# Kernel optimization log

Measured on AMD Instinct MI355X. Metric: run time of the kernel, lower is better.

The kernel has to match this reference:

```python
import jax, jax.numpy as jnp
import numpy as np


def _unfold(x, kh, kw):
    # torch.nn.functional.unfold ordering: channel-major, then kernel row, then kernel col
    B, C, H, W = x.shape
    Ho, Wo = H - kh + 1, W - kw + 1
    cols = jnp.stack([x[:, :, i:i + Ho, j:j + Wo]
                      for i in range(kh) for j in range(kw)], axis=2)  # [B,C,kh*kw,Ho,Wo]
    return cols.reshape(B, C * kh * kw, Ho * Wo), Ho, Wo


def _conv_unfold_matmul(x, w, b):
    # preprocessing: unfold -> A [B,L,K], B = w.view(O,-1).T [K,O]
    # matmul -> [B,L,O]; postprocessing: transpose, reshape, add bias
    O = w.shape[0]
    kh, kw = w.shape[2], w.shape[3]
    cols, Ho, Wo = _unfold(x, kh, kw)                      # [B,K,L]
    out = jnp.einsum('bkl,ok->bol', cols, w.reshape(O, -1))  # [B,O,L]
    return out.reshape(x.shape[0], O, Ho, Wo) + b[None, :, None, None]


def setup_inputs() -> dict:
    key = jax.random.key(0)
    ks = jax.random.split(key, 9)
    B = 4096
    x = jax.random.normal(ks[0], (B, 1, 28, 28), dtype=jnp.float32)
    w1 = jax.random.normal(ks[1], (10, 1, 10, 10), dtype=jnp.float32) * 0.1
    b1 = jax.random.normal(ks[2], (10,), dtype=jnp.float32) * 0.1
    w2 = jax.random.normal(ks[3], (20, 10, 10, 10), dtype=jnp.float32) * 0.03
    b2 = jax.random.normal(ks[4], (20,), dtype=jnp.float32) * 0.1
    w3 = jax.random.normal(ks[5], (20, 20, 5, 5), dtype=jnp.float32) * 0.04
    b3 = jax.random.normal(ks[6], (20,), dtype=jnp.float32) * 0.1
    wf = jax.random.normal(ks[7], (10, 720), dtype=jnp.float32) * 0.04
    bf = jax.random.normal(ks[8], (10,), dtype=jnp.float32) * 0.1
    return {"x": x, "w1": w1, "b1": b1, "w2": w2, "b2": b2,
            "w3": w3, "b3": b3, "wf": wf, "bf": bf}


def reference(x, w1, b1, w2, b2, w3, b3, wf, bf):
    h = jax.nn.relu(_conv_unfold_matmul(x, w1, b1))   # [B,10,19,19]
    h = jax.nn.relu(_conv_unfold_matmul(h, w2, b2))   # [B,20,10,10]
    h = jax.nn.relu(_conv_unfold_matmul(h, w3, b3))   # [B,20,6,6]
    h = h.reshape(-1, 720)
    return h @ wf.T + bf                               # [B,10]
```

## Files before the change

kernel.cpp:

```cpp
#include <hip/hip_runtime.h>


typedef short s16x4 __attribute__((ext_vector_type(4)));
typedef short s16x8 __attribute__((ext_vector_type(8)));
typedef float f32x4 __attribute__((ext_vector_type(4)));

#define ROW1 248
#define ROW2 248
#define XOFF 4712
#define SM_BYTES 11024

static __device__ __forceinline__ unsigned short f2bf(float f) {
    union { float f; unsigned int u; } v; v.f = f;
    unsigned int u = v.u;
    unsigned int r = (u + 0x7fffu + ((u >> 16) & 1u)) >> 16;
    return (unsigned short)r;
}

static __device__ __forceinline__ s16x8 cat8(s16x4 lo, s16x4 hi) {
    return __builtin_shufflevector(lo, hi, 0, 1, 2, 3, 4, 5, 6, 7);
}

__global__ __launch_bounds__(256) void wprep_k(const float* __restrict__ w1,
                                               const float* __restrict__ w2,
                                               const float* __restrict__ w3,
                                               unsigned short* __restrict__ wbuf) {
    int e = blockIdx.x * 256 + threadIdx.x;
    if (e < 40960) {
        int t = e & 7, lane = (e >> 3) & 63, nt = (e >> 9) & 1;
        int ck = (e >> 10) & 3, i = e >> 12;
        int k = ck * 32 + ((lane >> 4) & 3) * 8 + t;
        int o = nt * 16 + (lane & 15);
        int j = k / 12, c = k % 12;
        float val = (j < 10 && c < 10 && o < 20) ? w2[o * 1000 + c * 100 + i * 10 + j] : 0.f;
        wbuf[e] = f2bf(val);
    } else if (e < 61440) {
        int e2 = e - 40960;
        int t = e2 & 7, lane = (e2 >> 3) & 63, nt = (e2 >> 9) & 1;
        int ck = (e2 >> 10) & 3, i = e2 >> 12;
        int k = ck * 32 + ((lane >> 4) & 3) * 8 + t;
        int o = nt * 16 + (lane & 15);
        int j = k / 20, c = k % 20;
        float val = (j < 5 && o < 20) ? w3[o * 500 + c * 25 + i * 5 + j] : 0.f;
        wbuf[e] = f2bf(val);
    } else {
        int e2 = e - 61440;
        int t = e2 & 7, lane = (e2 >> 3) & 63;
        int kc = (e2 >> 9) % 9, nt = (e2 >> 9) / 9;
        int n = nt * 16 + (lane & 15);
        int k = kc * 32 + ((lane >> 4) & 3) * 8 + t;
        float val = 0.f;
        if (n < 190 && k < 280) {
            int ox = n / 10, o = n - ox * 10;
            int i = k / 28, xc = k - i * 28;
            int j = xc - ox;
            if (j >= 0 && j < 10) val = w1[o * 100 + i * 10 + j];
        }
        wbuf[61440 + e2] = f2bf(val);
    }
}

__global__ __launch_bounds__(128, 4) void fused_k(const float* __restrict__ x,
                                                  const float* __restrict__ b1,
                                                  const unsigned short* __restrict__ wbuf2,
                                                  const unsigned short* __restrict__ wbuf3,
                                                  const unsigned short* __restrict__ wband,
                                                  const float* __restrict__ b2,
                                                  const float* __restrict__ b3,
                                                  const float* __restrict__ wf,
                                                  const float* __restrict__ bf,
                                                  float* __restrict__ out) {
    __shared__ __align__(16) unsigned char smem[SM_BYTES];
    unsigned short* sm16 = (unsigned short*)smem;
    unsigned short* h1  = sm16;
    unsigned short* xbf = sm16 + XOFF;
    unsigned short* h2s = sm16;
    float*          h3s = (float*)smem;
    float*          fcp = (float*)(smem + 2880);

    const int tid = threadIdx.x;
    const int wave = tid >> 6, lane = tid & 63;
    const int b = blockIdx.x;
    const int quad = lane >> 4, lm = lane & 15;

    {
        const float4* src = (const float4*)(x + (size_t)b * 784);
        for (int k = tid; k < 196; k += 128) {
            float4 v = src[k];
            s16x4 p = { (short)f2bf(v.x), (short)f2bf(v.y),
                        (short)f2bf(v.z), (short)f2bf(v.w) };
            *(s16x4*)(xbf + k * 4) = p;
        }
        if (tid < 16) xbf[784 + tid] = 0;
        for (int e = tid; e < 95; e += 128) {
            int row = e / 5, seg = e - row * 5;
            *(s16x4*)(h1 + row * ROW1 + 228 + seg * 4) = (s16x4){0, 0, 0, 0};
        }
        for (int e = tid; e < 361; e += 128) {
            int oy = e / 19, ox = e - oy * 19;
            *(unsigned int*)(h1 + oy * ROW1 + ox * 12 + 10) = 0u;
        }
    }
    __syncthreads();

    {
        int m1 = lm + 16; if (m1 > 18) m1 = 18;
        const unsigned short* ab0 = xbf + lm * 28 + quad * 8;
        const unsigned short* ab1 = xbf + m1 * 28 + quad * 8;
        const unsigned short* wb = wband + lane * 8;
        f32x4 acc1[6][2] = {};
#pragma unroll
        for (int kc = 0; kc < 9; ++kc) {
            s16x8 a0 = cat8(*(const s16x4*)(ab0 + kc * 32),
                            *(const s16x4*)(ab0 + kc * 32 + 4));
            s16x8 a1 = cat8(*(const s16x4*)(ab1 + kc * 32),
                            *(const s16x4*)(ab1 + kc * 32 + 4));
#pragma unroll
            for (int q = 0; q < 6; ++q) {
                int nt = wave * 6 + q;
                s16x8 bw = *(const s16x8*)(wb + (nt * 9 + kc) * 512);
                acc1[q][0] = __builtin_amdgcn_mfma_f32_16x16x32_bf16(a0, bw, acc1[q][0], 0, 0, 0);
                acc1[q][1] = __builtin_amdgcn_mfma_f32_16x16x32_bf16(a1, bw, acc1[q][1], 0, 0, 0);
            }
        }
#pragma unroll
        for (int q = 0; q < 6; ++q) {
            int n = (wave * 6 + q) * 16 + lm;
            if (n < 190) {
                int ox = n / 10, o = n - ox * 10;
                float bias = b1[o];
#pragma unroll
                for (int mt = 0; mt < 2; ++mt) {
#pragma unroll
                    for (int r = 0; r < 4; ++r) {
                        int oy = mt * 16 + quad * 4 + r;
                        if (oy < 19)
                            h1[oy * ROW1 + ox * 12 + o] =
                                f2bf(fmaxf(acc1[q][mt][r] + bias, 0.f));
                    }
                }
            }
        }
    }
    __syncthreads();

    int abase[4];
#pragma unroll
    for (int mt = 0; mt < 4; ++mt) {
        int m = (wave * 4 + mt) * 16 + lm;
        if (m > 99) m = 99;
        int y = m / 10, xx = m - 10 * y;
        abase[mt] = y * ROW1 + xx * 12 + quad * 8;
    }
    f32x4 acc[4][2] = {};
    {
        const unsigned short* wptr = wbuf2 + lane * 8;
        s16x8 wc0 = *(const s16x8*)(wptr);
        s16x8 wc1 = *(const s16x8*)(wptr + 512);
#pragma unroll
        for (int it = 0; it < 40; ++it) {
            s16x8 wn0 = *(const s16x8*)(wptr + (it + 1) * 1024);
            s16x8 wn1 = *(const s16x8*)(wptr + (it + 1) * 1024 + 512);
            const unsigned short* sbi = h1 + (it >> 2) * ROW1 + (it & 3) * 32;
            s16x8 af[4];
#pragma unroll
            for (int mt = 0; mt < 4; ++mt) {
                const unsigned short* p = sbi + abase[mt];
                af[mt] = cat8(*(const s16x4*)(p), *(const s16x4*)(p + 4));
            }
#pragma unroll
            for (int mt = 0; mt < 4; ++mt) {
                acc[mt][0] = __builtin_amdgcn_mfma_f32_16x16x32_bf16(af[mt], wc0, acc[mt][0], 0, 0, 0);
                acc[mt][1] = __builtin_amdgcn_mfma_f32_16x16x32_bf16(af[mt], wc1, acc[mt][1], 0, 0, 0);
            }
            wc0 = wn0; wc1 = wn1;
        }
    }
    __syncthreads();

    for (int e = tid; e < 120; e += 128) {
        int row = e / 12, seg = e - row * 12;
        *(s16x4*)(h2s + row * ROW2 + 200 + seg * 4) = (s16x4){0, 0, 0, 0};
    }
#pragma unroll
    for (int mt = 0; mt < 4; ++mt) {
        int mtg = wave * 4 + mt;
        if (mtg < 7) {
#pragma unroll
            for (int nt = 0; nt < 2; ++nt) {
                int o = nt * 16 + lm;
                if (o < 20) {
                    float bias = b2[o];
#pragma unroll
                    for (int r = 0; r < 4; ++r) {
                        int pos = mtg * 16 + quad * 4 + r;
                        if (pos < 100) {
                            int y2 = pos / 10, x2 = pos - 10 * y2;
                            h2s[y2 * ROW2 + x2 * 20 + o] =
                                f2bf(fmaxf(acc[mt][nt][r] + bias, 0.f));
                        }
                    }
                }
            }
        }
    }
    __syncthreads();

    int abase3[2];
#pragma unroll
    for (int mt = 0; mt < 2; ++mt) {
        int m = (wave * 2 + mt) * 16 + lm;
        if (m > 35) m = 35;
        int oy = m / 6, ox = m - 6 * oy;
        abase3[mt] = oy * ROW2 + ox * 20 + quad * 8;
    }
    f32x4 acc3[2][2] = {};
    {
        const unsigned short* wptr = wbuf3 + lane * 8;
        s16x8 wc0 = *(const s16x8*)(wptr);
        s16x8 wc1 = *(const s16x8*)(wptr + 512);
#pragma unroll
        for (int it = 0; it < 20; ++it) {
            s16x8 wn0 = *(const s16x8*)(wptr + (it + 1) * 1024);
            s16x8 wn1 = *(const s16x8*)(wptr + (it + 1) * 1024 + 512);
            const unsigned short* sbi = h2s + (it >> 2) * ROW2 + (it & 3) * 32;
            s16x8 af[2];
#pragma unroll
            for (int mt = 0; mt < 2; ++mt) {
                const unsigned short* p = sbi + abase3[mt];
                af[mt] = cat8(*(const s16x4*)(p), *(const s16x4*)(p + 4));
            }
#pragma unroll
            for (int mt = 0; mt < 2; ++mt) {
                acc3[mt][0] = __builtin_amdgcn_mfma_f32_16x16x32_bf16(af[mt], wc0, acc3[mt][0], 0, 0, 0);
                acc3[mt][1] = __builtin_amdgcn_mfma_f32_16x16x32_bf16(af[mt], wc1, acc3[mt][1], 0, 0, 0);
            }
            wc0 = wn0; wc1 = wn1;
        }
    }
    __syncthreads();

#pragma unroll
    for (int mt = 0; mt < 2; ++mt) {
        int mtg = wave * 2 + mt;
        if (mtg < 3) {
#pragma unroll
            for (int nt = 0; nt < 2; ++nt) {
                int o = nt * 16 + lm;
                if (o < 20) {
                    float b3v = b3[o];
#pragma unroll
                    for (int r = 0; r < 4; ++r) {
                        int pos = mtg * 16 + quad * 4 + r;
                        if (pos < 36)
                            h3s[o * 36 + pos] = fmaxf(acc3[mt][nt][r] + b3v, 0.f);
                    }
                }
            }
        }
    }
    __syncthreads();

    float part[10];
#pragma unroll
    for (int n = 0; n < 10; ++n) part[n] = 0.f;
#pragma unroll 1
    for (int s = 0; s < 6; ++s) {
        int k = s * 128 + tid;
        if (k < 720) {
            float v = h3s[k];
#pragma unroll
            for (int n = 0; n < 10; ++n)
                part[n] = fmaf(v, wf[n * 720 + k], part[n]);
        }
    }
#pragma unroll
    for (int n = 0; n < 10; ++n) {
#pragma unroll
        for (int off = 32; off >= 1; off >>= 1)
            part[n] += __shfl_xor(part[n], off, 64);
    }
    if (lane == 0) {
#pragma unroll
        for (int n = 0; n < 10; ++n) fcp[wave * 10 + n] = part[n];
    }
    __syncthreads();
    if (tid < 10)
        out[(size_t)b * 10 + tid] = fcp[tid] + fcp[10 + tid] + bf[tid];
}

extern "C" void kernel_launch(void* const* d_in, const int* in_sizes, int n_in,
                              void* d_out, int out_size, void* d_ws, size_t ws_size,
                              hipStream_t stream) {
    (void)n_in; (void)out_size; (void)ws_size;
    const float* x  = (const float*)d_in[0];
    const float* w1 = (const float*)d_in[1];
    const float* b1 = (const float*)d_in[2];
    const float* w2 = (const float*)d_in[3];
    const float* b2 = (const float*)d_in[4];
    const float* w3 = (const float*)d_in[5];
    const float* b3 = (const float*)d_in[6];
    const float* wf = (const float*)d_in[7];
    const float* bf = (const float*)d_in[8];
    float* out = (float*)d_out;

    const int B = in_sizes[0] / 784;

    unsigned short* wbuf = (unsigned short*)d_ws;

    wprep_k<<<456, 256, 0, stream>>>(w1, w2, w3, wbuf);
    fused_k<<<B, 128, 0, stream>>>(x, b1, wbuf, wbuf + 40960, wbuf + 61440,
                                   b2, b3, wf, bf, out);
}
```

Before: 154.4 us.

## Double block size to four waves and software-pipeline LDS operand loads

Launches the fused per-sample kernel with 256 threads (4 waves) instead of 128, so each wave handles half as many output tiles in conv1, conv2 and conv3 and the FC reduction spans four partials. It also prefetches the next LDS A-fragment one iteration ahead in the conv2/conv3 MFMA loops. The intent is more waves per CU to hide latency and less register pressure per wave. The cost is idle waves in conv3, where only 3 of 4 waves have work, plus more barrier participants and possible occupancy limits from LDS or registers at 4 blocks of 256 threads.

```diff
diff --git a/kernel.cpp b/kernel.cpp
--- a/kernel.cpp
+++ b/kernel.cpp
@@ -60,7 +60,7 @@
     }
 }
 
-__global__ __launch_bounds__(128, 4) void fused_k(const float* __restrict__ x,
+__global__ __launch_bounds__(256, 4) void fused_k(const float* __restrict__ x,
                                                   const float* __restrict__ b1,
                                                   const unsigned short* __restrict__ wbuf2,
                                                   const unsigned short* __restrict__ wbuf3,
@@ -85,18 +85,18 @@
 
     {
         const float4* src = (const float4*)(x + (size_t)b * 784);
-        for (int k = tid; k < 196; k += 128) {
-            float4 v = src[k];
+        if (tid < 196) {
+            float4 v = src[tid];
             s16x4 p = { (short)f2bf(v.x), (short)f2bf(v.y),
                         (short)f2bf(v.z), (short)f2bf(v.w) };
-            *(s16x4*)(xbf + k * 4) = p;
+            *(s16x4*)(xbf + tid * 4) = p;
         }
         if (tid < 16) xbf[784 + tid] = 0;
-        for (int e = tid; e < 95; e += 128) {
-            int row = e / 5, seg = e - row * 5;
+        if (tid < 95) {
+            int row = tid / 5, seg = tid - row * 5;
             *(s16x4*)(h1 + row * ROW1 + 228 + seg * 4) = (s16x4){0, 0, 0, 0};
         }
-        for (int e = tid; e < 361; e += 128) {
+        for (int e = tid; e < 361; e += 256) {
             int oy = e / 19, ox = e - oy * 19;
             *(unsigned int*)(h1 + oy * ROW1 + ox * 12 + 10) = 0u;
         }
@@ -108,7 +108,7 @@
         const unsigned short* ab0 = xbf + lm * 28 + quad * 8;
         const unsigned short* ab1 = xbf + m1 * 28 + quad * 8;
         const unsigned short* wb = wband + lane * 8;
-        f32x4 acc1[6][2] = {};
+        f32x4 acc1[3][2] = {};
 #pragma unroll
         for (int kc = 0; kc < 9; ++kc) {
             s16x8 a0 = cat8(*(const s16x4*)(ab0 + kc * 32),
@@ -116,16 +116,16 @@
             s16x8 a1 = cat8(*(const s16x4*)(ab1 + kc * 32),
                             *(const s16x4*)(ab1 + kc * 32 + 4));
 #pragma unroll
-            for (int q = 0; q < 6; ++q) {
-                int nt = wave * 6 + q;
+            for (int q = 0; q < 3; ++q) {
+                int nt = wave * 3 + q;
                 s16x8 bw = *(const s16x8*)(wb + (nt * 9 + kc) * 512);
                 acc1[q][0] = __builtin_amdgcn_mfma_f32_16x16x32_bf16(a0, bw, acc1[q][0], 0, 0, 0);
                 acc1[q][1] = __builtin_amdgcn_mfma_f32_16x16x32_bf16(a1, bw, acc1[q][1], 0, 0, 0);
             }
         }
 #pragma unroll
-        for (int q = 0; q < 6; ++q) {
-            int n = (wave * 6 + q) * 16 + lm;
+        for (int q = 0; q < 3; ++q) {
+            int n = (wave * 3 + q) * 16 + lm;
             if (n < 190) {
                 int ox = n / 10, o = n - ox * 10;
                 float bias = b1[o];
@@ -144,48 +144,63 @@
     }
     __syncthreads();
 
-    int abase[4];
-#pragma unroll
-    for (int mt = 0; mt < 4; ++mt) {
-        int m = (wave * 4 + mt) * 16 + lm;
+    int abase[2];
+#pragma unroll
+    for (int mt = 0; mt < 2; ++mt) {
+        int tg = wave * 2 + mt; if (tg > 6) tg = 6;
+        int m = tg * 16 + lm;
         if (m > 99) m = 99;
         int y = m / 10, xx = m - 10 * y;
         abase[mt] = y * ROW1 + xx * 12 + quad * 8;
     }
-    f32x4 acc[4][2] = {};
+    f32x4 acc[2][2] = {};
     {
         const unsigned short* wptr = wbuf2 + lane * 8;
         s16x8 wc0 = *(const s16x8*)(wptr);
         s16x8 wc1 = *(const s16x8*)(wptr + 512);
+        s16x8 afc[2], afn[2];
+        {
+            const unsigned short* sbi = h1;
+            afc[0] = cat8(*(const s16x4*)(sbi + abase[0]),
+                          *(const s16x4*)(sbi + abase[0] + 4));
+            if (wave < 3)
+                afc[1] = cat8(*(const s16x4*)(sbi + abase[1]),
+                              *(const s16x4*)(sbi + abase[1] + 4));
+            else
+                afc[1] = afc[0];
+        }
 #pragma unroll
         for (int it = 0; it < 40; ++it) {
             s16x8 wn0 = *(const s16x8*)(wptr + (it + 1) * 1024);
             s16x8 wn1 = *(const s16x8*)(wptr + (it + 1) * 1024 + 512);
-            const unsigned short* sbi = h1 + (it >> 2) * ROW1 + (it & 3) * 32;
-            s16x8 af[4];
-#pragma unroll
-            for (int mt = 0; mt < 4; ++mt) {
-                const unsigned short* p = sbi + abase[mt];
-                af[mt] = cat8(*(const s16x4*)(p), *(const s16x4*)(p + 4));
-            }
-#pragma unroll
-            for (int mt = 0; mt < 4; ++mt) {
-                acc[mt][0] = __builtin_amdgcn_mfma_f32_16x16x32_bf16(af[mt], wc0, acc[mt][0], 0, 0, 0);
-                acc[mt][1] = __builtin_amdgcn_mfma_f32_16x16x32_bf16(af[mt], wc1, acc[mt][1], 0, 0, 0);
+            const unsigned short* sbn = h1 + ((it + 1) >> 2) * ROW1 + ((it + 1) & 3) * 32;
+            afn[0] = cat8(*(const s16x4*)(sbn + abase[0]),
+                          *(const s16x4*)(sbn + abase[0] + 4));
+            if (wave < 3)
+                afn[1] = cat8(*(const s16x4*)(sbn + abase[1]),
+                              *(const s16x4*)(sbn + abase[1] + 4));
+            else
+                afn[1] = afc[1];
+            acc[0][0] = __builtin_amdgcn_mfma_f32_16x16x32_bf16(afc[0], wc0, acc[0][0], 0, 0, 0);
+            acc[0][1] = __builtin_amdgcn_mfma_f32_16x16x32_bf16(afc[0], wc1, acc[0][1], 0, 0, 0);
+            if (wave < 3) {
+                acc[1][0] = __builtin_amdgcn_mfma_f32_16x16x32_bf16(afc[1], wc0, acc[1][0], 0, 0, 0);
+                acc[1][1] = __builtin_amdgcn_mfma_f32_16x16x32_bf16(afc[1], wc1, acc[1][1], 0, 0, 0);
             }
             wc0 = wn0; wc1 = wn1;
-        }
-    }
-    __syncthreads();
-
-    for (int e = tid; e < 120; e += 128) {
-        int row = e / 12, seg = e - row * 12;
+            afc[0] = afn[0]; afc[1] = afn[1];
+        }
+    }
+    __syncthreads();
+
+    if (tid < 120) {
+        int row = tid / 12, seg = tid - row * 12;
         *(s16x4*)(h2s + row * ROW2 + 200 + seg * 4) = (s16x4){0, 0, 0, 0};
     }
 #pragma unroll
-    for (int mt = 0; mt < 4; ++mt) {
-        int mtg = wave * 4 + mt;
-        if (mtg < 7) {
+    for (int mt = 0; mt < 2; ++mt) {
+        int tg = wave * 2 + mt;
+        if (tg < 7) {
 #pragma unroll
             for (int nt = 0; nt < 2; ++nt) {
                 int o = nt * 16 + lm;
@@ -193,7 +208,7 @@
                     float bias = b2[o];
 #pragma unroll
                     for (int r = 0; r < 4; ++r) {
-                        int pos = mtg * 16 + quad * 4 + r;
+                        int pos = tg * 16 + quad * 4 + r;
                         if (pos < 100) {
                             int y2 = pos / 10, x2 = pos - 10 * y2;
                             h2s[y2 * ROW2 + x2 * 20 + o] =
@@ -206,55 +221,42 @@
     }
     __syncthreads();
 
-    int abase3[2];
-#pragma unroll
-    for (int mt = 0; mt < 2; ++mt) {
-        int m = (wave * 2 + mt) * 16 + lm;
-        if (m > 35) m = 35;
+    f32x4 acc3[2] = {};
+    if (wave < 3) {
+        int m = wave * 16 + lm; if (m > 35) m = 35;
         int oy = m / 6, ox = m - 6 * oy;
-        abase3[mt] = oy * ROW2 + ox * 20 + quad * 8;
-    }
-    f32x4 acc3[2][2] = {};
-    {
+        const int ab3 = oy * ROW2 + ox * 20 + quad * 8;
         const unsigned short* wptr = wbuf3 + lane * 8;
         s16x8 wc0 = *(const s16x8*)(wptr);
         s16x8 wc1 = *(const s16x8*)(wptr + 512);
+        s16x8 afc = cat8(*(const s16x4*)(h2s + ab3),
+                         *(const s16x4*)(h2s + ab3 + 4));
 #pragma unroll
         for (int it = 0; it < 20; ++it) {
             s16x8 wn0 = *(const s16x8*)(wptr + (it + 1) * 1024);
             s16x8 wn1 = *(const s16x8*)(wptr + (it + 1) * 1024 + 512);
-            const unsigned short* sbi = h2s + (it >> 2) * ROW2 + (it & 3) * 32;
-            s16x8 af[2];
-#pragma unroll
-            for (int mt = 0; mt < 2; ++mt) {
-                const unsigned short* p = sbi + abase3[mt];
-                af[mt] = cat8(*(const s16x4*)(p), *(const s16x4*)(p + 4));
-            }
-#pragma unroll
-            for (int mt = 0; mt < 2; ++mt) {
-                acc3[mt][0] = __builtin_amdgcn_mfma_f32_16x16x32_bf16(af[mt], wc0, acc3[mt][0], 0, 0, 0);
-                acc3[mt][1] = __builtin_amdgcn_mfma_f32_16x16x32_bf16(af[mt], wc1, acc3[mt][1], 0, 0, 0);
-            }
+            const unsigned short* sbn = h2s + ((it + 1) >> 2) * ROW2 + ((it + 1) & 3) * 32;
+            s16x8 afn = cat8(*(const s16x4*)(sbn + ab3),
+                             *(const s16x4*)(sbn + ab3 + 4));
+            acc3[0] = __builtin_amdgcn_mfma_f32_16x16x32_bf16(afc, wc0, acc3[0], 0, 0, 0);
+            acc3[1] = __builtin_amdgcn_mfma_f32_16x16x32_bf16(afc, wc1, acc3[1], 0, 0, 0);
             wc0 = wn0; wc1 = wn1;
-        }
-    }
-    __syncthreads();
-
-#pragma unroll
-    for (int mt = 0; mt < 2; ++mt) {
-        int mtg = wave * 2 + mt;
-        if (mtg < 3) {
-#pragma unroll
-            for (int nt = 0; nt < 2; ++nt) {
-                int o = nt * 16 + lm;
-                if (o < 20) {
-                    float b3v = b3[o];
-#pragma unroll
-                    for (int r = 0; r < 4; ++r) {
-                        int pos = mtg * 16 + quad * 4 + r;
-                        if (pos < 36)
-                            h3s[o * 36 + pos] = fmaxf(acc3[mt][nt][r] + b3v, 0.f);
-                    }
+            afc = afn;
+        }
+    }
+    __syncthreads();
+
+    if (wave < 3) {
+#pragma unroll
+        for (int nt = 0; nt < 2; ++nt) {
+            int o = nt * 16 + lm;
+            if (o < 20) {
+                float b3v = b3[o];
+#pragma unroll
+                for (int r = 0; r < 4; ++r) {
+                    int pos = wave * 16 + quad * 4 + r;
+                    if (pos < 36)
+                        h3s[o * 36 + pos] = fmaxf(acc3[nt][r] + b3v, 0.f);
                 }
             }
         }
@@ -264,9 +266,9 @@
     float part[10];
 #pragma unroll
     for (int n = 0; n < 10; ++n) part[n] = 0.f;
-#pragma unroll 1
-    for (int s = 0; s < 6; ++s) {
-        int k = s * 128 + tid;
+#pragma unroll
+    for (int s = 0; s < 3; ++s) {
+        int k = s * 256 + tid;
         if (k < 720) {
             float v = h3s[k];
 #pragma unroll
@@ -286,7 +288,8 @@
     }
     __syncthreads();
     if (tid < 10)
-        out[(size_t)b * 10 + tid] = fcp[tid] + fcp[10 + tid] + bf[tid];
+        out[(size_t)b * 10 + tid] = fcp[tid] + fcp[10 + tid] + fcp[20 + tid]
+                                  + fcp[30 + tid] + bf[tid];
 }
 
 extern "C" void kernel_launch(void* const* d_in, const int* in_sizes, int n_in,
@@ -309,6 +312,6 @@
     unsigned short* wbuf = (unsigned short*)d_ws;
 
     wprep_k<<<456, 256, 0, stream>>>(w1, w2, w3, wbuf);
-    fused_k<<<B, 128, 0, stream>>>(x, b1, wbuf, wbuf + 40960, wbuf + 61440,
+    fused_k<<<B, 256, 0, stream>>>(x, b1, wbuf, wbuf + 40960, wbuf + 61440,
                                    b2, b3, wf, bf, out);
 }
```

Result: no change. 151.9 us (-1.6%).
